# Performance work log

Measured on AMD Instinct MI355X. Metric: run time of the kernel, lower is better.

The kernel has to match this reference:

```python
import jax, jax.numpy as jnp
import numpy as np

N_NODES = 20000
N_EDGES = 320000
MUL = 64            # multiplicity of 0e and 1o in hidden/out irreps
NUM_BASIS = 8
INV_SQRT3 = 0.5773502691896258
EPS = 1e-5


def setup_inputs() -> dict:
    key = jax.random.key(0)
    k = jax.random.split(key, 16)
    return {
        "node_hiddens": jax.random.normal(k[0], (N_NODES, 4 * MUL), dtype=jnp.float32),
        "edge_attr": jax.random.uniform(k[1], (N_EDGES, NUM_BASIS), dtype=jnp.float32),
        "edge_sh": jax.random.normal(k[2], (N_EDGES, 4), dtype=jnp.float32),
        "w1_s": jax.random.normal(k[3], (MUL, MUL), dtype=jnp.float32),
        "w1_v": jax.random.normal(k[4], (MUL, MUL), dtype=jnp.float32),
        "wsc_s": jax.random.normal(k[5], (MUL, MUL), dtype=jnp.float32),
        "wsc_v": jax.random.normal(k[6], (MUL, MUL), dtype=jnp.float32),
        "w2_s": jax.random.normal(k[7], (2 * MUL, MUL), dtype=jnp.float32),
        "w2_v": jax.random.normal(k[8], (2 * MUL, MUL), dtype=jnp.float32),
        "fc_w1": jax.random.normal(k[9], (NUM_BASIS, 64), dtype=jnp.float32),
        "fc_w2": jax.random.normal(k[10], (64, 64), dtype=jnp.float32),
        "fc_w3": jax.random.normal(k[11], (64, 4 * MUL), dtype=jnp.float32),
        "g_s": jnp.ones((MUL,), dtype=jnp.float32),
        "g_v": jnp.ones((MUL,), dtype=jnp.float32),
        "edge_index": jax.random.randint(k[12], (2, N_EDGES), 0, N_NODES),
    }


def reference(node_hiddens, edge_attr, edge_sh, w1_s, w1_v, wsc_s, wsc_v,
              w2_s, w2_v, fc_w1, fc_w2, fc_w3, g_s, g_v, edge_index):
    N = node_hiddens.shape[0]
    # e3nn layout: [N, 64x0e | 64x1o] with mul-major vectors
    xs = node_hiddens[:, :MUL]                        # [N, 64]
    xv = node_hiddens[:, MUL:].reshape(N, MUL, 3)     # [N, 64, 3]

    # edge MLP (FullyConnectedNet([8,64,64,256], silu)) -> per-edge TP weights
    h = jax.nn.silu(edge_attr @ fc_w1 * (1.0 / np.sqrt(float(NUM_BASIS))))
    h = jax.nn.silu(h @ fc_w2 * (1.0 / np.sqrt(64.0)))
    w = h @ fc_w3 * (1.0 / np.sqrt(64.0))             # [E, 4*MUL]
    wA, wB, wC, wD = jnp.split(w, 4, axis=1)          # one 64-vec per uvu path

    inv = 1.0 / np.sqrt(float(MUL))
    # self-connection Linear(hidden -> out)
    sc_s = xs @ wsc_s * inv
    sc_v = jnp.einsum('nud,uv->nvd', xv, wsc_v) * inv
    # linear_1 Linear(hidden -> hidden)
    ys = xs @ w1_s * inv
    yv = jnp.einsum('nud,uv->nvd', xv, w1_v) * inv

    src = edge_index[0]
    dst = edge_index[1]
    es = ys[dst]                                      # [E, 64] gather
    ev = yv[dst]                                      # [E, 64, 3]
    sh0 = edge_sh[:, :1]                              # [E, 1]
    sh1 = edge_sh[:, 1:]                              # [E, 3]

    # weighted uvu Clebsch-Gordan tensor product -> irreps_mid (sorted order)
    m0a = wA * es * sh0                                          # 0e x 0e -> 0e
    m0b = wD * jnp.einsum('eud,ed->eu', ev, sh1) * INV_SQRT3     # 1o x 1o -> 0e
    m1a = wB[:, :, None] * es[:, :, None] * sh1[:, None, :]      # 0e x 1o -> 1o
    m1b = wC[:, :, None] * ev * sh0[:, :, None]                  # 1o x 0e -> 1o
    mid_s = jnp.concatenate([m0a, m0b], axis=1)       # [E, 128]
    mid_v = jnp.concatenate([m1a, m1b], axis=1)       # [E, 128, 3]

    # scatter-sum to source nodes + 1/sqrt(degree) normalization
    ns = jax.ops.segment_sum(mid_s, src, num_segments=N)
    nv = jax.ops.segment_sum(mid_v, src, num_segments=N)
    deg = jax.ops.segment_sum(jnp.ones((src.shape[0],), node_hiddens.dtype), src, num_segments=N)
    dn = jax.lax.rsqrt(jnp.maximum(deg, 1.0))
    ns = ns * dn[:, None]
    nv = nv * dn[:, None, None]

    # linear_2 Linear(128x0e+128x1o -> 64x0e+64x1o) + self connection
    inv2 = 1.0 / np.sqrt(2.0 * MUL)
    os_ = ns @ w2_s * inv2 + sc_s
    ov = jnp.einsum('nud,uv->nvd', nv, w2_v) * inv2 + sc_v

    # equivariant RMS layer norm per irrep type (centering=False)
    os_ = os_ * jax.lax.rsqrt(jnp.mean(os_ * os_, axis=1, keepdims=True) + EPS) * g_s
    rms_v = jax.lax.rsqrt(jnp.mean(ov * ov, axis=(1, 2))[:, None, None] + EPS)
    ov = ov * rms_v * g_v[None, :, None]

    return jnp.concatenate([os_, ov.reshape(N, 3 * MUL)], axis=1)
```

## Files before the change

### kernel.cpp

```cpp
#include <hip/hip_runtime.h>
#include <math.h>

#define N_NODES 20000
#define N_EDGES 320000
#define N_TILES 1250

typedef __attribute__((ext_vector_type(8))) short bf16x8;
typedef __attribute__((ext_vector_type(4))) float f32x4;
typedef __attribute__((ext_vector_type(2))) unsigned u32x2;
typedef __attribute__((ext_vector_type(4))) unsigned u32x4;

__device__ __forceinline__ float silu_f(float x) {
    return x / (1.0f + __expf(-x));
}
__device__ __forceinline__ short f2bf(float x) {
    union { float f; unsigned u; } v; v.f = x;
    unsigned r = (v.u + 0x7FFFu + ((v.u >> 16) & 1u)) >> 16;
    return (short)r;
}
__device__ __forceinline__ float blo(unsigned u) { return __uint_as_float(u << 16); }
__device__ __forceinline__ float bhi(unsigned u) { return __uint_as_float(u & 0xFFFF0000u); }
__device__ __forceinline__ unsigned cvt_pk(float lo, float hi) {
    unsigned r;
    asm("v_cvt_pk_bf16_f32 %0, %1, %2" : "=v"(r) : "v"(lo), "v"(hi));
    return r;
}
__device__ __forceinline__ float rlane(float v, int l) {
    return __uint_as_float(__builtin_amdgcn_readlane(__float_as_uint(v), l));
}
#define MFMA16(a, b, c) __builtin_amdgcn_mfma_f32_16x16x32_bf16((a), (b), (c), 0, 0, 0)

__global__ __launch_bounds__(256) void s_hist(const int* __restrict__ eidx,
                                              int* __restrict__ cnt) {
    const int e = blockIdx.x * 256 + threadIdx.x;
    if (e < N_EDGES) atomicAdd(&cnt[eidx[e]], 1);
}

__global__ __launch_bounds__(1024) void s_scan(int* __restrict__ cnt,
                                               int* __restrict__ start) {
    const int tid = threadIdx.x;
    const int base = tid * 20;
    int vals[20];
    int sum = 0;
    #pragma unroll
    for (int j = 0; j < 20; ++j) {
        const int i = base + j;
        const int v = (i < N_NODES) ? cnt[i] : 0;
        vals[j] = sum;
        sum += v;
    }
    const int lane = tid & 63, wv = tid >> 6;
    int x = sum;
    #pragma unroll
    for (int off = 1; off < 64; off <<= 1) {
        const int t = __shfl_up(x, off);
        if (lane >= off) x += t;
    }
    __shared__ int wtot[16];
    if (lane == 63) wtot[wv] = x;
    __syncthreads();
    int wpref = 0;
    for (int k = 0; k < wv; ++k) wpref += wtot[k];
    const int excl = wpref + x - sum;
    #pragma unroll
    for (int j = 0; j < 20; ++j) {
        const int i = base + j;
        if (i < N_NODES) {
            const int s = excl + vals[j];
            start[i] = s;
            cnt[i] = s;
        }
    }
    if (tid == 1023) start[N_NODES] = wpref + x;
}

__global__ __launch_bounds__(256) void s_scatter(const int* __restrict__ eidx,
                                                 const float* __restrict__ esh,
                                                 int* __restrict__ cursor,
                                                 int* __restrict__ perm,
                                                 int* __restrict__ dst_perm,
                                                 float* __restrict__ esh_perm) {
    const int e = blockIdx.x * 256 + threadIdx.x;
    if (e >= N_EDGES) return;
    const int src = eidx[e];
    const int pos = atomicAdd(&cursor[src], 1);
    perm[pos] = e;
    dst_perm[pos] = eidx[N_EDGES + e];
    *(float4*)(esh_perm + (size_t)pos * 4) = *(const float4*)(esh + (size_t)e * 4);
}

__global__ __launch_bounds__(256) void k_pack(
    const float* __restrict__ fcw1, const float* __restrict__ fcw2,
    const float* __restrict__ fcw3,
    const float* __restrict__ w1s, const float* __restrict__ wscs,
    const float* __restrict__ w1v, const float* __restrict__ wscv,
    const float* __restrict__ w2s, const float* __restrict__ w2v,
    short* __restrict__ w1A, short* __restrict__ w2A, short* __restrict__ w3A,
    short* __restrict__ wp1, short* __restrict__ wp2)
{
    const int tid = blockIdx.x * 256 + threadIdx.x;
    const int nthr = gridDim.x * 256;
    for (int i = tid; i < 4*64*8; i += nthr) {
        const int j = i & 7, lane = (i >> 3) & 63, t = i >> 9;
        const int k = (lane >> 4) * 8 + j, row = t*16 + (lane & 15);
        w1A[i] = (k < 8) ? f2bf(fcw1[k*64 + row]) : (short)0;
    }
    for (int i = tid; i < 8*64*8; i += nthr) {
        const int j = i & 7, lane = (i >> 3) & 63, kk = (i >> 9) & 1, t = i >> 10;
        const int k = kk*32 + (lane >> 4)*8 + j, row = t*16 + (lane & 15);
        w2A[i] = f2bf(fcw2[k*64 + row]);
    }
    for (int i = tid; i < 32*64*8; i += nthr) {
        const int j = i & 7, lane = (i >> 3) & 63, kk = (i >> 9) & 1, T = i >> 10;
        const int k = kk*32 + (lane >> 4)*8 + j, c = T*16 + (lane & 15);
        const float s = (c >= 192) ? 0.5773502691896258f : 1.0f;
        w3A[i] = f2bf(fcw3[(size_t)k*256 + c] * s);
    }
    for (int i = tid; i < 4096; i += nthr) {
        const int j = i & 7, lane = (i >> 3) & 63, kk = (i >> 9) & 1, vt = i >> 10;
        const int row = vt*16 + (lane & 15), k = kk*32 + (lane >> 4)*8 + j;
        wp1[i]         = f2bf(w1s [k*64 + row]);
        wp1[4096 + i]  = f2bf(wscs[k*64 + row]);
        wp1[8192 + i]  = f2bf(w1v [k*64 + row]);
        wp1[12288 + i] = f2bf(wscv[k*64 + row]);
    }
    for (int i = tid; i < 8192; i += nthr) {
        const int j = i & 7, lane = (i >> 3) & 63, kk = (i >> 9) & 3, vt = i >> 11;
        const int row = vt*16 + (lane & 15), k = kk*32 + (lane >> 4)*8 + j;
        const int r = (k & 1)*64 + (k >> 1);
        wp2[i]        = f2bf(w2s[r*64 + row]);
        wp2[8192 + i] = f2bf(w2v[r*64 + row]);
    }
}

__global__ __launch_bounds__(256) void k1_mfma(
    const float* __restrict__ nh, const short* __restrict__ wp1,
    short* __restrict__ ydata, short* __restrict__ scpack)
{
    const int lane = threadIdx.x & 63;
    const int tile = blockIdx.x * 4 + (threadIdx.x >> 6);
    if (tile >= N_TILES) return;
    const int l15 = lane & 15, lhi = lane >> 4;
    const int n = tile*16 + l15;
    const float* row = nh + (size_t)n * 256;
    const f32x4 zz = {0.f, 0.f, 0.f, 0.f};
    f32x4 acc[8][4];
    #pragma unroll
    for (int c = 0; c < 8; ++c)
        #pragma unroll
        for (int vt = 0; vt < 4; ++vt) acc[c][vt] = zz;

    #pragma unroll
    for (int kk = 0; kk < 2; ++kk) {
        const int k0 = kk*32 + lhi*8;
        const float4 s0 = *(const float4*)(row + k0);
        const float4 s1 = *(const float4*)(row + k0 + 4);
        float4 vv[6];
        #pragma unroll
        for (int q = 0; q < 6; ++q) vv[q] = *(const float4*)(row + 64 + 3*k0 + q*4);
        const float* vf = (const float*)vv;
        union { u32x4 u; bf16x8 v; } bs, b0, b1, b2;
        bs.u[0] = cvt_pk(s0.x, s0.y); bs.u[1] = cvt_pk(s0.z, s0.w);
        bs.u[2] = cvt_pk(s1.x, s1.y); bs.u[3] = cvt_pk(s1.z, s1.w);
        #pragma unroll
        for (int q = 0; q < 4; ++q) {
            b0.u[q] = cvt_pk(vf[6*q + 0], vf[6*q + 3]);
            b1.u[q] = cvt_pk(vf[6*q + 1], vf[6*q + 4]);
            b2.u[q] = cvt_pk(vf[6*q + 2], vf[6*q + 5]);
        }
        #pragma unroll
        for (int vt = 0; vt < 4; ++vt) {
            const int fo = ((vt*2 + kk)*64 + lane)*8;
            const bf16x8 a_ys = *(const bf16x8*)&wp1[fo];
            const bf16x8 a_ss = *(const bf16x8*)&wp1[4096 + fo];
            const bf16x8 a_yv = *(const bf16x8*)&wp1[8192 + fo];
            const bf16x8 a_sv = *(const bf16x8*)&wp1[12288 + fo];
            acc[0][vt] = MFMA16(a_ys, bs.v, acc[0][vt]);
            acc[1][vt] = MFMA16(a_ss, bs.v, acc[1][vt]);
            acc[2][vt] = MFMA16(a_yv, b0.v, acc[2][vt]);
            acc[3][vt] = MFMA16(a_yv, b1.v, acc[3][vt]);
            acc[4][vt] = MFMA16(a_yv, b2.v, acc[4][vt]);
            acc[5][vt] = MFMA16(a_sv, b0.v, acc[5][vt]);
            acc[6][vt] = MFMA16(a_sv, b1.v, acc[6][vt]);
            acc[7][vt] = MFMA16(a_sv, b2.v, acc[7][vt]);
        }
    }
    #pragma unroll
    for (int vt = 0; vt < 4; ++vt)
        #pragma unroll
        for (int r = 0; r < 4; ++r) {
            const int v = vt*16 + lhi*4 + r;
            u32x2 yo, so;
            yo[0] = cvt_pk(acc[0][vt][r]*0.125f, acc[2][vt][r]*0.125f);
            yo[1] = cvt_pk(acc[3][vt][r]*0.125f, acc[4][vt][r]*0.125f);
            so[0] = cvt_pk(acc[1][vt][r]*0.125f, acc[5][vt][r]*0.125f);
            so[1] = cvt_pk(acc[6][vt][r]*0.125f, acc[7][vt][r]*0.125f);
            *(u32x2*)&ydata [((size_t)n*64 + v)*4] = yo;
            *(u32x2*)&scpack[((size_t)n*64 + v)*4] = so;
        }
}

__global__ __launch_bounds__(256) void k_mlp(
    const float* __restrict__ ea, const int* __restrict__ perm,
    const short* __restrict__ w1A, const short* __restrict__ w2A,
    const short* __restrict__ w3A, short* __restrict__ wq)
{
    __shared__ short hb1[4][1024];
    __shared__ short hb2[4][1024];
    __shared__ short wslab[4][4096];
    const int lane = threadIdx.x & 63, w = threadIdx.x >> 6;
    const int l15 = lane & 15, lhi = lane >> 4;
    const int wbase = (blockIdx.x * 4 + w) * 64;
    short* h1b = hb1[w];
    short* h2b = hb2[w];
    short* slab = wslab[w];
    const int swz = (l15 & 7) << 4;
    const f32x4 zz = {0.f, 0.f, 0.f, 0.f};

    bf16x8 a1[4], a2[4][2];
    #pragma unroll
    for (int t = 0; t < 4; ++t)
        a1[t] = *(const bf16x8*)&w1A[(t*64 + lane)*8];
    #pragma unroll
    for (int t = 0; t < 4; ++t)
        #pragma unroll
        for (int kk = 0; kk < 2; ++kk)
            a2[t][kk] = *(const bf16x8*)&w2A[((t*2 + kk)*64 + lane)*8];

    for (int sb = 0; sb < 4; ++sb) {
        bf16x8 bea = {0,0,0,0,0,0,0,0};
        if (lhi == 0) {
            const int e = perm[wbase + sb*16 + l15];
            const float4 p0 = *(const float4*)(ea + (size_t)e*8);
            const float4 p1 = *(const float4*)(ea + (size_t)e*8 + 4);
            union { u32x4 u; bf16x8 v; } tu;
            tu.u[0] = cvt_pk(p0.x, p0.y);
            tu.u[1] = cvt_pk(p0.z, p0.w);
            tu.u[2] = cvt_pk(p1.x, p1.y);
            tu.u[3] = cvt_pk(p1.z, p1.w);
            bea = tu.v;
        }
        f32x4 d1[4];
        #pragma unroll
        for (int t = 0; t < 4; ++t)
            d1[t] = MFMA16(a1[t], bea, zz);
        #pragma unroll
        for (int t = 0; t < 4; ++t) {
            const float s0 = silu_f(d1[t][0] * 0.35355339059327373f);
            const float s1 = silu_f(d1[t][1] * 0.35355339059327373f);
            const float s2 = silu_f(d1[t][2] * 0.35355339059327373f);
            const float s3 = silu_f(d1[t][3] * 0.35355339059327373f);
            u32x2 pk; pk[0] = cvt_pk(s0, s1); pk[1] = cvt_pk(s2, s3);
            const int byt = (l15*128 + t*32 + lhi*8) ^ swz;
            *(u32x2*)((char*)h1b + byt) = pk;
        }
        bf16x8 bh1[2];
        #pragma unroll
        for (int kk = 0; kk < 2; ++kk)
            bh1[kk] = *(const bf16x8*)((const char*)h1b + ((l15*128 + kk*64 + lhi*16) ^ swz));
        f32x4 d2[4];
        #pragma unroll
        for (int t = 0; t < 4; ++t) {
            d2[t] = MFMA16(a2[t][0], bh1[0], zz);
            d2[t] = MFMA16(a2[t][1], bh1[1], d2[t]);
        }
        #pragma unroll
        for (int t = 0; t < 4; ++t) {
            const float s0 = silu_f(d2[t][0] * 0.125f) * 0.125f;
            const float s1 = silu_f(d2[t][1] * 0.125f) * 0.125f;
            const float s2 = silu_f(d2[t][2] * 0.125f) * 0.125f;
            const float s3 = silu_f(d2[t][3] * 0.125f) * 0.125f;
            u32x2 pk; pk[0] = cvt_pk(s0, s1); pk[1] = cvt_pk(s2, s3);
            const int byt = (l15*128 + t*32 + lhi*8) ^ swz;
            *(u32x2*)((char*)h2b + byt) = pk;
        }
        bf16x8 bh2[2];
        #pragma unroll
        for (int kk = 0; kk < 2; ++kk)
            bh2[kk] = *(const bf16x8*)((const char*)h2b + ((l15*128 + kk*64 + lhi*16) ^ swz));

        #pragma unroll
        for (int T = 0; T < 16; ++T) {
            const bf16x8 a30 = *(const bf16x8*)&w3A[((T*2 + 0)*64 + lane)*8];
            const bf16x8 a31 = *(const bf16x8*)&w3A[((T*2 + 1)*64 + lane)*8];
            f32x4 d = MFMA16(a30, bh2[0], zz);
            d = MFMA16(a31, bh2[1], d);
            const int g = T >> 2;
            const int vb = (T & 3)*16 + lhi*4;
            const unsigned p01 = cvt_pk(d[0], d[1]);
            const unsigned p23 = cvt_pk(d[2], d[3]);
            short* sl = slab + l15*256;
            const int m = l15 & 7;
            sl[(((vb + 0) ^ m) << 2) + g] = (short)(p01 & 0xFFFFu);
            sl[(((vb + 1) ^ m) << 2) + g] = (short)(p01 >> 16);
            sl[(((vb + 2) ^ m) << 2) + g] = (short)(p23 & 0xFFFFu);
            sl[(((vb + 3) ^ m) << 2) + g] = (short)(p23 >> 16);
        }

        #pragma unroll
        for (int i = 0; i < 16; ++i) {
            const u32x2 wv = *(const u32x2*)(slab + i*256 + ((lane ^ (i & 7)) << 2));
            const int slot = wbase + sb*16 + i;
            *(u32x2*)&wq[((size_t)slot*64 + lane)*4] = wv;
        }
    }
}

__global__ __launch_bounds__(256) void k2_gather(
    const int* __restrict__ start, const int* __restrict__ dst_perm,
    const float* __restrict__ esh_perm, const short* __restrict__ wq,
    const short* __restrict__ ydata, unsigned* __restrict__ ncat32)
{
    const int lane = threadIdx.x & 63;
    const int n = blockIdx.x * 4 + (threadIdx.x >> 6);
    if (n >= N_NODES) return;
    const int s0 = start[n], s1 = start[n + 1];
    float acc0=0.f, acc1=0.f, av0=0.f, av1=0.f, av2=0.f, bv0=0.f, bv1=0.f, bv2=0.f;
    for (int p = s0; p < s1; p += 8) {
        const int m = s1 - p;
        u32x2 wv[8], yd[8];
        float4 sh[8];
        #pragma unroll
        for (int j = 0; j < 8; ++j) {
            const int pp = (j < m) ? p + j : s0;
            wv[j] = *(const u32x2*)&wq[((size_t)pp*64 + lane)*4];
            sh[j] = *(const float4*)(esh_perm + (size_t)pp*4);
            const int dst = dst_perm[pp];
            yd[j] = *(const u32x2*)&ydata[((size_t)dst*64 + lane)*4];
        }
        #pragma unroll
        for (int j = 0; j < 8; ++j) {
            const float g = (j < m) ? 1.f : 0.f;
            const float wa = blo(wv[j][0])*g, wb = bhi(wv[j][0])*g;
            const float wc = blo(wv[j][1])*g, wd = bhi(wv[j][1])*g;
            const float es  = blo(yd[j][0]), ev0 = bhi(yd[j][0]);
            const float ev1 = blo(yd[j][1]), ev2 = bhi(yd[j][1]);
            acc0 += wa * es * sh[j].x;
            acc1 += wd * (ev0*sh[j].y + ev1*sh[j].z + ev2*sh[j].w);
            const float esb = wb * es;
            av0 += esb * sh[j].y; av1 += esb * sh[j].z; av2 += esb * sh[j].w;
            const float c0 = wc * sh[j].x;
            bv0 += c0 * ev0; bv1 += c0 * ev1; bv2 += c0 * ev2;
        }
    }
    unsigned* nrow = ncat32 + (size_t)n * 256;
    nrow[lane]        = cvt_pk(acc0, acc1);
    nrow[64  + lane]  = cvt_pk(av0, bv0);
    nrow[128 + lane]  = cvt_pk(av1, bv1);
    nrow[192 + lane]  = cvt_pk(av2, bv2);
}

__global__ __launch_bounds__(256) void k3_mfma(
    const unsigned* __restrict__ ncat32, const int* __restrict__ start,
    const short* __restrict__ wp2, const short* __restrict__ scpack,
    const float* __restrict__ gs, const float* __restrict__ gv,
    float* __restrict__ out)
{
    const int lane = threadIdx.x & 63;
    const int tile = blockIdx.x * 4 + (threadIdx.x >> 6);
    if (tile >= N_TILES) return;
    const int l15 = lane & 15, lhi = lane >> 4;
    const int n = tile*16 + l15;
    const f32x4 zz = {0.f, 0.f, 0.f, 0.f};
    f32x4 acc[4][4];
    #pragma unroll
    for (int c = 0; c < 4; ++c)
        #pragma unroll
        for (int vt = 0; vt < 4; ++vt) acc[c][vt] = zz;

    const size_t nb = (size_t)n * 256;
    #pragma unroll
    for (int kk = 0; kk < 4; ++kk) {
        const int uo = kk*16 + lhi*4;
        union { u32x4 u; bf16x8 v; } bs, b0, b1, b2;
        bs.u = *(const u32x4*)&ncat32[nb +        uo];
        b0.u = *(const u32x4*)&ncat32[nb +  64 + uo];
        b1.u = *(const u32x4*)&ncat32[nb + 128 + uo];
        b2.u = *(const u32x4*)&ncat32[nb + 192 + uo];
        #pragma unroll
        for (int vt = 0; vt < 4; ++vt) {
            const int fo = ((vt*4 + kk)*64 + lane)*8;
            const bf16x8 a_s = *(const bf16x8*)&wp2[fo];
            const bf16x8 a_v = *(const bf16x8*)&wp2[8192 + fo];
            acc[0][vt] = MFMA16(a_s, bs.v, acc[0][vt]);
            acc[1][vt] = MFMA16(a_v, b0.v, acc[1][vt]);
            acc[2][vt] = MFMA16(a_v, b1.v, acc[2][vt]);
            acc[3][vt] = MFMA16(a_v, b2.v, acc[3][vt]);
        }
    }
    const float degf = (float)(start[n+1] - start[n]);
    const float coef = rsqrtf(fmaxf(degf, 1.0f)) * 0.08838834764831845f;
    float os[4][4], o0[4][4], o1[4][4], o2[4][4];
    float ssq = 0.f, vsq = 0.f;
    #pragma unroll
    for (int vt = 0; vt < 4; ++vt)
        #pragma unroll
        for (int r = 0; r < 4; ++r) {
            const int v = vt*16 + lhi*4 + r;
            const u32x2 sc = *(const u32x2*)&scpack[((size_t)n*64 + v)*4];
            os[vt][r] = acc[0][vt][r]*coef + blo(sc[0]);
            o0[vt][r] = acc[1][vt][r]*coef + bhi(sc[0]);
            o1[vt][r] = acc[2][vt][r]*coef + blo(sc[1]);
            o2[vt][r] = acc[3][vt][r]*coef + bhi(sc[1]);
            ssq += os[vt][r]*os[vt][r];
            vsq += o0[vt][r]*o0[vt][r] + o1[vt][r]*o1[vt][r] + o2[vt][r]*o2[vt][r];
        }
    ssq += __shfl_xor(ssq, 16); ssq += __shfl_xor(ssq, 32);
    vsq += __shfl_xor(vsq, 16); vsq += __shfl_xor(vsq, 32);
    const float rs = rsqrtf(ssq * (1.0f/64.0f) + 1e-5f);
    const float rv = rsqrtf(vsq * (1.0f/192.0f) + 1e-5f);
    float* orow = out + (size_t)n * 256;
    #pragma unroll
    for (int vt = 0; vt < 4; ++vt) {
        const int vb = vt*16 + lhi*4;
        const float4 g4  = *(const float4*)(gs + vb);
        const float4 gv4 = *(const float4*)(gv + vb);
        const float4 so = { os[vt][0]*rs*g4.x, os[vt][1]*rs*g4.y,
                            os[vt][2]*rs*g4.z, os[vt][3]*rs*g4.w };
        *(float4*)(orow + vb) = so;
        const float m0 = rv*gv4.x, m1 = rv*gv4.y, m2 = rv*gv4.z, m3 = rv*gv4.w;
        const float4 w0 = { o0[vt][0]*m0, o1[vt][0]*m0, o2[vt][0]*m0, o0[vt][1]*m1 };
        const float4 w1 = { o1[vt][1]*m1, o2[vt][1]*m1, o0[vt][2]*m2, o1[vt][2]*m2 };
        const float4 w2 = { o2[vt][2]*m2, o0[vt][3]*m3, o1[vt][3]*m3, o2[vt][3]*m3 };
        float* vbase = orow + 64 + vb*3;
        *(float4*)(vbase)     = w0;
        *(float4*)(vbase + 4) = w1;
        *(float4*)(vbase + 8) = w2;
    }
}

extern "C" void kernel_launch(void* const* d_in, const int* in_sizes, int n_in,
                              void* d_out, int out_size, void* d_ws, size_t ws_size,
                              hipStream_t stream) {
    const float* nh   = (const float*)d_in[0];
    const float* ea   = (const float*)d_in[1];
    const float* esh  = (const float*)d_in[2];
    const float* w1s  = (const float*)d_in[3];
    const float* w1v  = (const float*)d_in[4];
    const float* wscs = (const float*)d_in[5];
    const float* wscv = (const float*)d_in[6];
    const float* w2s  = (const float*)d_in[7];
    const float* w2v  = (const float*)d_in[8];
    const float* fcw1 = (const float*)d_in[9];
    const float* fcw2 = (const float*)d_in[10];
    const float* fcw3 = (const float*)d_in[11];
    const float* gs   = (const float*)d_in[12];
    const float* gv   = (const float*)d_in[13];
    const int*   eidx = (const int*)d_in[14];
    float* out = (float*)d_out;

    char* wsb = (char*)d_ws;
    size_t off = 0;
    short* ydata  = (short*)(wsb + off); off += (size_t)N_NODES * 256 * 2;
    short* scpack = (short*)(wsb + off); off += (size_t)N_NODES * 256 * 2;
    unsigned* ncat32 = (unsigned*)(wsb + off); off += (size_t)N_NODES * 256 * 4;
    float* esh_perm  = (float*)(wsb + off); off += (size_t)N_EDGES * 4 * 4;
    int* cnt      = (int*)(wsb + off); off += (size_t)N_NODES * 4;
    int* start    = (int*)(wsb + off); off += ((size_t)N_NODES + 1) * 4;
    int* perm     = (int*)(wsb + off); off += (size_t)N_EDGES * 4;
    int* dst_perm = (int*)(wsb + off); off += (size_t)N_EDGES * 4;
    short* w1A = (short*)(wsb + off); off += 2048 * 2;
    short* w2A = (short*)(wsb + off); off += 4096 * 2;
    short* w3A = (short*)(wsb + off); off += 16384 * 2;
    short* wp1 = (short*)(wsb + off); off += 16384 * 2;
    short* wp2 = (short*)(wsb + off); off += 16384 * 2;
    off = (off + 15) & ~(size_t)15;
    short* wq = (short*)(wsb + off);

    hipMemsetAsync(cnt, 0, N_NODES * sizeof(int), stream);

    s_hist<<<(N_EDGES + 255)/256, 256, 0, stream>>>(eidx, cnt);
    s_scan<<<1, 1024, 0, stream>>>(cnt, start);
    s_scatter<<<(N_EDGES + 255)/256, 256, 0, stream>>>(
        eidx, esh, cnt, perm, dst_perm, esh_perm);

    k_pack<<<32, 256, 0, stream>>>(fcw1, fcw2, fcw3, w1s, wscs, w1v, wscv,
                                   w2s, w2v, w1A, w2A, w3A, wp1, wp2);

    k1_mfma<<<(N_TILES + 3)/4, 256, 0, stream>>>(nh, wp1, ydata, scpack);

    k_mlp<<<N_EDGES/256, 256, 0, stream>>>(ea, perm, w1A, w2A, w3A, wq);

    k2_gather<<<(N_NODES + 3)/4, 256, 0, stream>>>(
        start, dst_perm, esh_perm, wq, ydata, ncat32);

    k3_mfma<<<(N_TILES + 3)/4, 256, 0, stream>>>(
        ncat32, start, wp2, scpack, gs, gv, out);
}
```

Baseline: 249.3 us.

## Reorder fc_w3 packing so MLP writes per-edge weights directly without LDS slab

Repacks fc_w3 tiles so that each group of four MFMA outputs holds the four weight groups for the same channel. The MLP kernel can then pack them into 8-byte stores straight to global memory, removing the LDS transpose slab and its scattered 2-byte stores. Each wave now handles 32 edges instead of 64, with twice as many blocks, and each w3A fragment load is reused across two 16-edge sub-batches. Global stores are now strided per lane rather than contiguous per row, which could hurt coalescing.

```diff
diff --git a/kernel.cpp b/kernel.cpp
--- a/kernel.cpp
+++ b/kernel.cpp
@@ -24,9 +24,6 @@
     unsigned r;
     asm("v_cvt_pk_bf16_f32 %0, %1, %2" : "=v"(r) : "v"(lo), "v"(hi));
     return r;
-}
-__device__ __forceinline__ float rlane(float v, int l) {
-    return __uint_as_float(__builtin_amdgcn_readlane(__float_as_uint(v), l));
 }
 #define MFMA16(a, b, c) __builtin_amdgcn_mfma_f32_16x16x32_bf16((a), (b), (c), 0, 0, 0)
 
@@ -111,10 +108,12 @@
         w2A[i] = f2bf(fcw2[k*64 + row]);
     }
     for (int i = tid; i < 32*64*8; i += nthr) {
-        const int j = i & 7, lane = (i >> 3) & 63, kk = (i >> 9) & 1, T = i >> 10;
-        const int k = kk*32 + (lane >> 4)*8 + j, c = T*16 + (lane & 15);
-        const float s = (c >= 192) ? 0.5773502691896258f : 1.0f;
-        w3A[i] = f2bf(fcw3[(size_t)k*256 + c] * s);
+        const int j = i & 7, lane = (i >> 3) & 63, kk = (i >> 9) & 1, Tp = i >> 10;
+        const int c = Tp >> 2, q = Tp & 3;
+        const int k = kk*32 + (lane >> 4)*8 + j;
+        const int ch = (q*4 + c)*16 + (lane & 15);
+        const float s = (ch >= 192) ? 0.5773502691896258f : 1.0f;
+        w3A[i] = f2bf(fcw3[(size_t)k*256 + ch] * s);
     }
     for (int i = tid; i < 4096; i += nthr) {
         const int j = i & 7, lane = (i >> 3) & 63, kk = (i >> 9) & 1, vt = i >> 10;
@@ -207,13 +206,11 @@
 {
     __shared__ short hb1[4][1024];
     __shared__ short hb2[4][1024];
-    __shared__ short wslab[4][4096];
     const int lane = threadIdx.x & 63, w = threadIdx.x >> 6;
     const int l15 = lane & 15, lhi = lane >> 4;
-    const int wbase = (blockIdx.x * 4 + w) * 64;
+    const int wbase = (blockIdx.x * 4 + w) * 32;
     short* h1b = hb1[w];
     short* h2b = hb2[w];
-    short* slab = wslab[w];
     const int swz = (l15 & 7) << 4;
     const f32x4 zz = {0.f, 0.f, 0.f, 0.f};
 
@@ -227,7 +224,9 @@
         for (int kk = 0; kk < 2; ++kk)
             a2[t][kk] = *(const bf16x8*)&w2A[((t*2 + kk)*64 + lane)*8];
 
-    for (int sb = 0; sb < 4; ++sb) {
+    bf16x8 bh2[2][2];
+    #pragma unroll
+    for (int sb = 0; sb < 2; ++sb) {
         bf16x8 bea = {0,0,0,0,0,0,0,0};
         if (lhi == 0) {
             const int e = perm[wbase + sb*16 + l15];
@@ -274,34 +273,36 @@
             const int byt = (l15*128 + t*32 + lhi*8) ^ swz;
             *(u32x2*)((char*)h2b + byt) = pk;
         }
-        bf16x8 bh2[2];
         #pragma unroll
         for (int kk = 0; kk < 2; ++kk)
-            bh2[kk] = *(const bf16x8*)((const char*)h2b + ((l15*128 + kk*64 + lhi*16) ^ swz));
-
-        #pragma unroll
-        for (int T = 0; T < 16; ++T) {
-            const bf16x8 a30 = *(const bf16x8*)&w3A[((T*2 + 0)*64 + lane)*8];
-            const bf16x8 a31 = *(const bf16x8*)&w3A[((T*2 + 1)*64 + lane)*8];
-            f32x4 d = MFMA16(a30, bh2[0], zz);
-            d = MFMA16(a31, bh2[1], d);
-            const int g = T >> 2;
-            const int vb = (T & 3)*16 + lhi*4;
-            const unsigned p01 = cvt_pk(d[0], d[1]);
-            const unsigned p23 = cvt_pk(d[2], d[3]);
-            short* sl = slab + l15*256;
-            const int m = l15 & 7;
-            sl[(((vb + 0) ^ m) << 2) + g] = (short)(p01 & 0xFFFFu);
-            sl[(((vb + 1) ^ m) << 2) + g] = (short)(p01 >> 16);
-            sl[(((vb + 2) ^ m) << 2) + g] = (short)(p23 & 0xFFFFu);
-            sl[(((vb + 3) ^ m) << 2) + g] = (short)(p23 >> 16);
-        }
-
-        #pragma unroll
-        for (int i = 0; i < 16; ++i) {
-            const u32x2 wv = *(const u32x2*)(slab + i*256 + ((lane ^ (i & 7)) << 2));
-            const int slot = wbase + sb*16 + i;
-            *(u32x2*)&wq[((size_t)slot*64 + lane)*4] = wv;
+            bh2[sb][kk] = *(const bf16x8*)((const char*)h2b + ((l15*128 + kk*64 + lhi*16) ^ swz));
+    }
+
+    #pragma unroll
+    for (int c = 0; c < 4; ++c) {
+        f32x4 dq[4][2];
+        #pragma unroll
+        for (int q = 0; q < 4; ++q) {
+            const int Tp = c*4 + q;
+            const bf16x8 a30 = *(const bf16x8*)&w3A[((Tp*2 + 0)*64 + lane)*8];
+            const bf16x8 a31 = *(const bf16x8*)&w3A[((Tp*2 + 1)*64 + lane)*8];
+            #pragma unroll
+            for (int sb = 0; sb < 2; ++sb) {
+                f32x4 d = MFMA16(a30, bh2[sb][0], zz);
+                dq[q][sb] = MFMA16(a31, bh2[sb][1], d);
+            }
+        }
+        #pragma unroll
+        for (int sb = 0; sb < 2; ++sb) {
+            const int slot = wbase + sb*16 + l15;
+            #pragma unroll
+            for (int r = 0; r < 4; ++r) {
+                const int v = c*16 + lhi*4 + r;
+                u32x2 pk;
+                pk[0] = cvt_pk(dq[0][sb][r], dq[1][sb][r]);
+                pk[1] = cvt_pk(dq[2][sb][r], dq[3][sb][r]);
+                *(u32x2*)&wq[((size_t)slot*64 + v)*4] = pk;
+            }
         }
     }
 }
@@ -479,7 +480,7 @@
 
     k1_mfma<<<(N_TILES + 3)/4, 256, 0, stream>>>(nh, wp1, ydata, scpack);
 
-    k_mlp<<<N_EDGES/256, 256, 0, stream>>>(ea, perm, w1A, w2A, w3A, wq);
+    k_mlp<<<N_EDGES/128, 256, 0, stream>>>(ea, perm, w1A, w2A, w3A, wq);
 
     k2_gather<<<(N_NODES + 3)/4, 256, 0, stream>>>(
         start, dst_perm, esh_perm, wq, ydata, ncat32);
```

Result: faster. 220.9 us (-11.4%).
